# Kernel optimization log

Hardware: AMD Instinct MI355X
Metric: run time of the kernel (lower is better)

## Reference

```python
import jax, jax.numpy as jnp
import numpy as np

NUM_HEADS = 12


def get_rel_pos(q_size, k_size, rel_pos):
    # rel_pos: (2*max(q,k)-1, head_dim); sizes match table here so no resize.
    max_rel_dist = int(2 * max(q_size, k_size) - 1)
    if rel_pos.shape[0] != max_rel_dist:
        rel_pos = jax.image.resize(rel_pos, (max_rel_dist, rel_pos.shape[1]), method='linear')
    q_coords = jnp.arange(q_size)[:, None] * max(k_size / q_size, 1.0)
    k_coords = jnp.arange(k_size)[None, :] * max(q_size / k_size, 1.0)
    rel = (q_coords - k_coords + (k_size - 1) * max(q_size / k_size, 1.0)).astype(jnp.int32)
    return rel_pos[rel.reshape(-1)].reshape(q_size, k_size, -1)  # (q, k, head_dim)


def setup_inputs() -> dict:
    key = jax.random.key(0)
    ks = jax.random.split(key, 7)
    B, H, W, C = 8, 32, 32, 768
    head_dim = C // NUM_HEADS
    return {
        'x': jax.random.normal(ks[0], (B, H, W, C), jnp.float32),
        'w_qkv': jax.random.normal(ks[1], (C, 3 * C), jnp.float32) * 0.02,
        'b_qkv': jnp.zeros((3 * C,), jnp.float32),
        'rel_pos_h': jax.random.normal(ks[2], (2 * H - 1, head_dim), jnp.float32) * 0.02,
        'rel_pos_w': jax.random.normal(ks[3], (2 * W - 1, head_dim), jnp.float32) * 0.02,
        'w_proj': jax.random.normal(ks[4], (C, C), jnp.float32) * 0.02,
        'b_proj': jnp.zeros((C,), jnp.float32),
    }


def reference(x, w_qkv, b_qkv, rel_pos_h, rel_pos_w, w_proj, b_proj):
    B, H, W, C = x.shape
    heads = NUM_HEADS
    hd = C // heads
    S = H * W
    qkv = x @ w_qkv + b_qkv                                  # (B,H,W,3C)
    qkv = qkv.reshape(B, S, 3, heads, hd).transpose(2, 0, 3, 1, 4)
    qkv = qkv.reshape(3, B * heads, S, hd)
    q, k, v = qkv[0], qkv[1], qkv[2]
    attn = (q * hd ** -0.5) @ k.transpose(0, 2, 1)           # (B*heads, S, S)
    rh = get_rel_pos(H, H, rel_pos_h)                        # (H,H,hd)
    rw = get_rel_pos(W, W, rel_pos_w)                        # (W,W,hd)
    r_q = q.reshape(B * heads, H, W, hd)
    rel_h = jnp.einsum('bhwc,hkc->bhwk', r_q, rh)
    rel_w = jnp.einsum('bhwc,wkc->bhwk', r_q, rw)
    attn = (attn.reshape(B * heads, H, W, H, W)
            + rel_h[:, :, :, :, None]
            + rel_w[:, :, :, None, :]).reshape(B * heads, S, S)
    attn = jax.nn.softmax(attn, axis=-1)
    out = (attn @ v).reshape(B, heads, H, W, hd).transpose(0, 2, 3, 1, 4).reshape(B, H, W, C)
    return out @ w_proj + b_proj
```

## Files before the change

kernel.cpp:

```cpp
#include <hip/hip_runtime.h>
#include <hip/hip_bf16.h>

#define BATCH 8
#define SEQ   1024
#define CH    768
#define NH    12
#define HD    64
#define BH    96
#define N_QKV 2304

#define LOG2E 1.44269504088896f

typedef __attribute__((ext_vector_type(8))) short bfrag;
typedef __attribute__((ext_vector_type(4))) short short4v;
typedef __attribute__((ext_vector_type(4))) float ffrag;
typedef __attribute__((ext_vector_type(4))) int  intv4;
typedef __attribute__((ext_vector_type(2))) int  intv2;

__device__ __forceinline__ short f2bf(float x) {
    __hip_bfloat16 h = __float2bfloat16(x);
    return *reinterpret_cast<short*>(&h);
}
__device__ __forceinline__ float bf2f(short b) {
    __hip_bfloat16 h;
    *reinterpret_cast<short*>(&h) = b;
    return __bfloat162float(h);
}
__device__ __forceinline__ void split2(float x, short& hi, short& lo) {
    short h = f2bf(x);
    hi = h;
    lo = f2bf(x - bf2f(h));
}
__device__ __forceinline__ void async_copy16(void* lds, const void* g) {
    __builtin_amdgcn_global_load_lds(
        (const __attribute__((address_space(1))) void*)g,
        (__attribute__((address_space(3))) void*)lds, 16, 0, 0);
}
__device__ __forceinline__ void pinned_load16(intv4& dst, const void* p) {
    asm volatile("global_load_dwordx4 %0, %1, off"
                 : "=&v"(dst) : "v"((unsigned long long)p));
}

__global__ __launch_bounds__(256) void prep(
    const float* __restrict__ x,
    const float* __restrict__ w_qkv, const float* __restrict__ w_proj,
    short* __restrict__ Xh,
    short* __restrict__ WqhT,
    short* __restrict__ WphT, short* __restrict__ WplT)
{
    __shared__ float ts[32][33];
    const int tid = threadIdx.x;
    const int bid = blockIdx.x;

    if (bid < 512) {
        const int n4 = (BATCH * SEQ * CH) / 4;
        for (int i = bid * 256 + tid; i < n4; i += 512 * 256) {
            float4 f = ((const float4*)x)[i];
            short4v h;
            h[0] = f2bf(f.x); h[1] = f2bf(f.y); h[2] = f2bf(f.z); h[3] = f2bf(f.w);
            ((short4v*)Xh)[i] = h;
        }
        return;
    }
    if (bid < 2240) {
        int t = bid - 512;
        const int bx = t % 72, by = t / 72;
        const int r0 = by * 32, c0 = bx * 32;
        #pragma unroll
        for (int i = 0; i < 4; ++i) {
            int idx = tid + i * 256;
            int rr = idx >> 5, cc = idx & 31;
            ts[rr][cc] = w_qkv[(size_t)(r0 + rr) * N_QKV + c0 + cc];
        }
        __syncthreads();
        #pragma unroll
        for (int i = 0; i < 4; ++i) {
            int idx = tid + i * 256;
            int rr = idx >> 5, cc = idx & 31;
            WqhT[(size_t)(c0 + rr) * CH + r0 + cc] = f2bf(ts[cc][rr]);
        }
        return;
    }
    {
        int t = bid - 2240;
        const int bx = t % 24, by = t / 24;
        const int r0 = by * 32, c0 = bx * 32;
        #pragma unroll
        for (int i = 0; i < 4; ++i) {
            int idx = tid + i * 256;
            int rr = idx >> 5, cc = idx & 31;
            ts[rr][cc] = w_proj[(size_t)(r0 + rr) * CH + c0 + cc];
        }
        __syncthreads();
        #pragma unroll
        for (int i = 0; i < 4; ++i) {
            int idx = tid + i * 256;
            int rr = idx >> 5, cc = idx & 31;
            short h, l;
            split2(ts[cc][rr], h, l);
            WphT[(size_t)(c0 + rr) * CH + r0 + cc] = h;
            WplT[(size_t)(c0 + rr) * CH + r0 + cc] = l;
        }
    }
}

__global__ __launch_bounds__(256) void gemm_qkv_mfma(
    const short* __restrict__ Xh,
    const short* __restrict__ WhT,
    const float* __restrict__ bias,
    short* __restrict__ qh, short* __restrict__ kh, short* __restrict__ vT)
{
    __shared__ short lds[2 * 12288];
    const int id  = blockIdx.x;
    const int xcd = id & 7;
    const int per = id >> 3;
    const int mi_ = per & 3;
    const int ni_ = per >> 2;
    const int m0 = (xcd * 4 + mi_) * 256;
    const int n0 = ni_ * 128;
    const int which = n0 / CH;

    const int tid = threadIdx.x;
    const int wave = tid >> 6, lane = tid & 63;
    const int quad = lane >> 4, l16 = lane & 15;

    const size_t srow = (size_t)(tid >> 2) * CH
                      + (size_t)((tid & 3) ^ ((tid >> 3) & 3)) * 8;
    const short* asrc = Xh  + (size_t)m0 * CH + srow;
    const short* bsrc = WhT + (size_t)n0 * CH + srow;

    const int xs = (quad ^ ((l16 >> 1) & 3)) * 8;

    ffrag acc[4][8];
    #pragma unroll
    for (int i = 0; i < 4; ++i)
        #pragma unroll
        for (int j = 0; j < 8; ++j) acc[i][j] = (ffrag){0.f, 0.f, 0.f, 0.f};

    #pragma unroll
    for (int i = 0; i < 4; ++i)
        async_copy16(lds + i * 2048 + tid * 8, asrc + (size_t)i * 64 * CH);
    #pragma unroll
    for (int i = 0; i < 2; ++i)
        async_copy16(lds + 8192 + i * 2048 + tid * 8, bsrc + (size_t)i * 64 * CH);

    for (int c = 0; c < 24; ++c) {
        const int cur = c & 1;
        if (c < 23) {
            short* w = lds + (cur ^ 1) * 12288;
            #pragma unroll
            for (int i = 0; i < 4; ++i)
                async_copy16(w + i * 2048 + tid * 8,
                             asrc + (size_t)i * 64 * CH + (c + 1) * 32);
            #pragma unroll
            for (int i = 0; i < 2; ++i)
                async_copy16(w + 8192 + i * 2048 + tid * 8,
                             bsrc + (size_t)i * 64 * CH + (c + 1) * 32);
            asm volatile("s_waitcnt vmcnt(6)");
        } else {
            asm volatile("s_waitcnt vmcnt(0)");
        }
        __builtin_amdgcn_s_barrier();
        __builtin_amdgcn_sched_barrier(0);

        const short* Ab = lds + cur * 12288;
        const short* Bb = Ab + 8192;
        bfrag ah[4], bh[8];
        #pragma unroll
        for (int i = 0; i < 4; ++i)
            ah[i] = *(const bfrag*)&Ab[(wave * 64 + i * 16 + l16) * 32 + xs];
        #pragma unroll
        for (int j = 0; j < 8; ++j)
            bh[j] = *(const bfrag*)&Bb[(j * 16 + l16) * 32 + xs];
        __builtin_amdgcn_s_setprio(1);
        #pragma unroll
        for (int mi = 0; mi < 4; ++mi)
            #pragma unroll
            for (int ni = 0; ni < 8; ++ni)
                acc[mi][ni] = __builtin_amdgcn_mfma_f32_16x16x32_bf16(
                    ah[mi], bh[ni], acc[mi][ni], 0, 0, 0);
        __builtin_amdgcn_s_setprio(0);

        __builtin_amdgcn_s_barrier();
    }

    const int b = m0 >> 10;
    #pragma unroll
    for (int ni = 0; ni < 8; ++ni) {
        int n = n0 + ni * 16 + l16;
        float bv = bias[n];
        int nin = n - which * CH;
        int head = nin >> 6, d = nin & 63;
        #pragma unroll
        for (int mi = 0; mi < 4; ++mi) {
            if (which == 2) {
                int s_base = (m0 & 1023) + wave * 64 + mi * 16 + quad * 4;
                short4v pk;
                #pragma unroll
                for (int r = 0; r < 4; ++r) pk[r] = f2bf(acc[mi][ni][r] + bv);
                *(short4v*)&vT[((size_t)(b * NH + head) * HD + d) * SEQ + s_base] = pk;
            } else {
                const float scale = (which == 0) ? 0.125f * LOG2E : 1.0f;
                short* dst = (which == 0) ? qh : kh;
                #pragma unroll
                for (int r = 0; r < 4; ++r) {
                    int m = m0 + wave * 64 + mi * 16 + quad * 4 + r;
                    int s = m & 1023;
                    dst[((size_t)(b * NH + head) * SEQ + s) * HD + d] =
                        f2bf((acc[mi][ni][r] + bv) * scale);
                }
            }
        }
    }
}

__device__ __forceinline__ void gemm_core3(
    short* lds,
    const short* __restrict__ Ah, const short* __restrict__ Al,
    const short* __restrict__ BhT, const short* __restrict__ BlT,
    int m0, int n0, ffrag acc[4][4])
{
    const int tid = threadIdx.x;
    const int wave = tid >> 6, lane = tid & 63;
    const int quad = lane >> 4, l16 = lane & 15;
    const int wm = (wave & 1) * 64, wn = (wave >> 1) * 64;

    const short* src;
    int row0;
    if (wave == 0)      { src = Ah;  row0 = m0; }
    else if (wave == 1) { src = Al;  row0 = m0; }
    else if (wave == 2) { src = BhT; row0 = n0; }
    else                { src = BlT; row0 = n0; }
    const size_t lane_off = (size_t)(lane >> 2) * CH
                          + (size_t)((lane & 3) ^ ((lane >> 3) & 3)) * 8;
    const short* sbase = src + (size_t)row0 * CH + lane_off;
    short* wsec = lds + wave * 4096;

    const int xs = (quad ^ ((l16 >> 1) & 3)) * 8;

    #pragma unroll
    for (int i = 0; i < 8; ++i)
        async_copy16(wsec + i * 512, sbase + (size_t)i * 16 * CH);

    for (int c = 0; c < 24; ++c) {
        const int cur = c & 1;
        if (c < 23) {
            short* w = wsec + (cur ^ 1) * 16384;
            #pragma unroll
            for (int i = 0; i < 8; ++i)
                async_copy16(w + i * 512,
                             sbase + (size_t)i * 16 * CH + (c + 1) * 32);
            asm volatile("s_waitcnt vmcnt(8)");
        } else {
            asm volatile("s_waitcnt vmcnt(0)");
        }
        __builtin_amdgcn_s_barrier();
        __builtin_amdgcn_sched_barrier(0);

        const short* base = lds + cur * 16384;
        bfrag ah[4], al[4], bh[4], bl[4];
        #pragma unroll
        for (int i = 0; i < 4; ++i) {
            int ra = (wm + i * 16 + l16) * 32 + xs;
            int rb = (wn + i * 16 + l16) * 32 + xs;
            ah[i] = *(const bfrag*)&base[ra];
            al[i] = *(const bfrag*)&base[4096 + ra];
            bh[i] = *(const bfrag*)&base[8192 + rb];
            bl[i] = *(const bfrag*)&base[12288 + rb];
        }
        #pragma unroll
        for (int mi = 0; mi < 4; ++mi)
            #pragma unroll
            for (int ni = 0; ni < 4; ++ni) {
                acc[mi][ni] = __builtin_amdgcn_mfma_f32_16x16x32_bf16(ah[mi], bh[ni], acc[mi][ni], 0, 0, 0);
                acc[mi][ni] = __builtin_amdgcn_mfma_f32_16x16x32_bf16(ah[mi], bl[ni], acc[mi][ni], 0, 0, 0);
                acc[mi][ni] = __builtin_amdgcn_mfma_f32_16x16x32_bf16(al[mi], bh[ni], acc[mi][ni], 0, 0, 0);
            }

        __builtin_amdgcn_s_barrier();
    }
}

__global__ __launch_bounds__(256) void gemm_proj_mfma(
    const short* __restrict__ Ah, const short* __restrict__ Al,
    const short* __restrict__ WhT, const short* __restrict__ WlT,
    const float* __restrict__ bias, float* __restrict__ out)
{
    __shared__ short lds[2 * 16384];
    const int id  = blockIdx.x;
    const int xcd = id & 7;
    const int per = id >> 3;
    const int mi_ = per & 7;
    const int ni_ = per >> 3;
    const int m0 = (xcd * 8 + mi_) * 128;
    const int n0 = ni_ * 128;

    ffrag acc[4][4];
    #pragma unroll
    for (int i = 0; i < 4; ++i)
        #pragma unroll
        for (int j = 0; j < 4; ++j) acc[i][j] = (ffrag){0.f, 0.f, 0.f, 0.f};

    gemm_core3(lds, Ah, Al, WhT, WlT, m0, n0, acc);

    const int tid = threadIdx.x;
    const int wave = tid >> 6, lane = tid & 63;
    const int quad = lane >> 4, l16 = lane & 15;
    const int wm = (wave & 1) * 64, wn = (wave >> 1) * 64;

    #pragma unroll
    for (int ni = 0; ni < 4; ++ni) {
        int n = n0 + wn + ni * 16 + l16;
        float bv = bias[n];
        #pragma unroll
        for (int mi = 0; mi < 4; ++mi)
            #pragma unroll
            for (int r = 0; r < 4; ++r) {
                int m = m0 + wm + mi * 16 + quad * 4 + r;
                out[(size_t)m * CH + n] = acc[mi][ni][r] + bv;
            }
    }
}

__global__ __launch_bounds__(256, 3) void attn_kernel(
    const short* __restrict__ qh,
    const short* __restrict__ kh_g, const short* __restrict__ vT_g,
    const float* __restrict__ rph,
    const float* __restrict__ rpw,
    short* __restrict__ aoh, short* __restrict__ aol)
{
    const int fid   = blockIdx.x;
    const int xcd   = fid & 7;
    const int inner = fid >> 3;
    const int s0    = (inner & 7) * 128;
    const int bh    = xcd * 12 + (inner >> 3);

    const int tid  = threadIdx.x;
    const int wave = tid >> 6;
    const int lane = tid & 63;
    const int quad = lane >> 4;
    const int l16  = lane & 15;

    __shared__ short Kh[64 * 64];
    __shared__ short Vth[64 * 64];
    __shared__ short Th[128][68];
    __shared__ short Tw_Ps[128 * 68];

    const size_t bh_koff = (size_t)bh * SEQ * HD;
    const size_t bh_voff = (size_t)bh * HD * SEQ;
    const size_t klane = (size_t)(lane >> 3) * HD + (size_t)((lane & 7) ^ (lane >> 3)) * 8;

    const short* kbase = kh_g + bh_koff + klane;
    const int i0 = wave * 2;
    short* KhW0 = Kh + i0 * 512 + lane * 8;

    const short* vgbase = vT_g + bh_voff
        + (size_t)(wave * 16 + (lane >> 3)) * SEQ + (size_t)(lane & 7) * 8;

    int vwA[2], vwB[2];
    {
        const int m  = lane & 7;
        const int oA = ((m >> 2) << 2) + ((m & 1) << 1);
        const int hf = (m >> 1) & 1;
        #pragma unroll
        for (int jj = 0; jj < 2; ++jj) {
            int d = wave * 16 + jj * 8 + (lane >> 3);
            vwA[jj] = d * 64 + ((oA ^ (d & 7)) << 3) + hf * 4;
            vwB[jj] = d * 64 + (((oA + 1) ^ (d & 7)) << 3) + hf * 4;
        }
    }

    intv4 kA0, kA1, vA0, vA1, kB0, kB1, vB0, vB1;
    pinned_load16(kA0, kbase + (size_t)(i0 * 8) * HD);
    pinned_load16(kA1, kbase + (size_t)(i0 * 8 + 8) * HD);
    pinned_load16(vA0, vgbase);
    pinned_load16(vA1, vgbase + (size_t)8 * SEQ);

    bfrag qfh[2][2];
    #pragma unroll
    for (int g = 0; g < 2; ++g) {
        const size_t qrow = ((size_t)bh * SEQ + s0 + wave * 32 + g * 16 + l16) * HD;
        #pragma unroll
        for (int kc = 0; kc < 2; ++kc)
            qfh[g][kc] = *(const bfrag*)(qh + qrow + kc * 32 + quad * 8);
    }

    #pragma unroll
    for (int table = 0; table < 2; ++table) {
        const float* tbl = table ? rpw : rph;
        #pragma unroll
        for (int n0r = 0; n0r < 64; n0r += 16) {
            int r = n0r + l16;
            bfrag bfr[2];
            #pragma unroll
            for (int kc = 0; kc < 2; ++kc) {
                if (r < 63) {
                    const float* trow = tbl + (size_t)r * HD + kc * 32 + quad * 8;
                    float4 f0 = *(const float4*)(trow);
                    float4 f1 = *(const float4*)(trow + 4);
                    float xs[8] = {f0.x, f0.y, f0.z, f0.w, f1.x, f1.y, f1.z, f1.w};
                    #pragma unroll
                    for (int j = 0; j < 8; ++j) bfr[kc][j] = f2bf(xs[j]);
                } else {
                    #pragma unroll
                    for (int j = 0; j < 8; ++j) bfr[kc][j] = 0;
                }
            }
            #pragma unroll
            for (int g = 0; g < 2; ++g) {
                ffrag acc = {0.f, 0.f, 0.f, 0.f};
                acc = __builtin_amdgcn_mfma_f32_16x16x32_bf16(qfh[g][0], bfr[0], acc, 0, 0, 0);
                acc = __builtin_amdgcn_mfma_f32_16x16x32_bf16(qfh[g][1], bfr[1], acc, 0, 0, 0);
                int row = wave * 32 + g * 16 + quad * 4;
                #pragma unroll
                for (int reg = 0; reg < 4; ++reg) {
                    short v = f2bf(acc[reg] * 8.0f);
                    if (table) Tw_Ps[(row + reg) * 68 + n0r + l16] = v;
                    else       Th[row + reg][n0r + l16] = v;
                }
            }
        }
    }

    float tw_r[2][2][4];
    #pragma unroll
    for (int g = 0; g < 2; ++g) {
        int qloc = wave * 32 + g * 16 + l16;
        int wq = g * 16 + l16;
        #pragma unroll
        for (int p = 0; p < 2; ++p)
            #pragma unroll
            for (int reg = 0; reg < 4; ++reg)
                tw_r[g][p][reg] = bf2f(Tw_Ps[qloc * 68 + (wq - (p * 16 + quad * 4 + reg) + 31)]);
    }
    const int hq_w = (s0 >> 5) + wave;

    float l_part[2] = {0.f, 0.f};
    ffrag Ot[2][4];
    #pragma unroll
    for (int g = 0; g < 2; ++g)
        #pragma unroll
        for (int t = 0; t < 4; ++t) Ot[g][t] = (ffrag){0.f, 0.f, 0.f, 0.f};

    auto chunk = [&](int c, const intv4& ck0, const intv4& ck1,
                     const intv4& cv0, const intv4& cv1,
                     intv4& nk0, intv4& nk1, intv4& nv0, intv4& nv1) {
        __syncthreads();
        if (c < 15) {
            const int cn = c + 1;
            pinned_load16(nk0, kbase + (size_t)(cn * 64 + i0 * 8) * HD);
            pinned_load16(nk1, kbase + (size_t)(cn * 64 + i0 * 8 + 8) * HD);
            pinned_load16(nv0, vgbase + cn * 64);
            pinned_load16(nv1, vgbase + (size_t)8 * SEQ + cn * 64);
            asm volatile("s_waitcnt vmcnt(4)");
        } else {
            asm volatile("s_waitcnt vmcnt(0)");
        }
        __builtin_amdgcn_sched_barrier(0);
        *(intv4*)KhW0         = ck0;
        *(intv4*)(KhW0 + 512) = ck1;
        {
            intv2 lo0 = {cv0[0], cv0[1]}, hi0 = {cv0[2], cv0[3]};
            intv2 lo1 = {cv1[0], cv1[1]}, hi1 = {cv1[2], cv1[3]};
            *(intv2*)&Vth[vwA[0]] = lo0;
            *(intv2*)&Vth[vwB[0]] = hi0;
            *(intv2*)&Vth[vwA[1]] = lo1;
            *(intv2*)&Vth[vwB[1]] = hi1;
        }
        __syncthreads();

        float th_r[2][2];
        #pragma unroll
        for (int g = 0; g < 2; ++g) {
            int qloc = wave * 32 + g * 16 + l16;
            th_r[g][0] = bf2f(Th[qloc][hq_w - 2 * c + 31]);
            th_r[g][1] = bf2f(Th[qloc][hq_w - 2 * c - 1 + 31]);
        }

        #pragma unroll
        for (int ktp = 0; ktp < 2; ++ktp) {
            bfrag kbhE[2], kbhO[2];
            #pragma unroll
            for (int kc = 0; kc < 2; ++kc) {
                int xs = ((kc * 4 + quad) ^ (l16 & 7)) * 8;
                kbhE[kc] = *(const bfrag*)&Kh[((2 * ktp) * 16 + l16) * 64 + xs];
                kbhO[kc] = *(const bfrag*)&Kh[((2 * ktp + 1) * 16 + l16) * 64 + xs];
            }
            bfrag pf[2];
            #pragma unroll
            for (int g = 0; g < 2; ++g) {
                ffrag aE, aO;
                #pragma unroll
                for (int reg = 0; reg < 4; ++reg) {
                    aE[reg] = th_r[g][ktp] + tw_r[g][0][reg];
                    aO[reg] = th_r[g][ktp] + tw_r[g][1][reg];
                }
                __builtin_amdgcn_s_setprio(1);
                aE = __builtin_amdgcn_mfma_f32_16x16x32_bf16(kbhE[0], qfh[g][0], aE, 0, 0, 0);
                aE = __builtin_amdgcn_mfma_f32_16x16x32_bf16(kbhE[1], qfh[g][1], aE, 0, 0, 0);
                aO = __builtin_amdgcn_mfma_f32_16x16x32_bf16(kbhO[0], qfh[g][0], aO, 0, 0, 0);
                aO = __builtin_amdgcn_mfma_f32_16x16x32_bf16(kbhO[1], qfh[g][1], aO, 0, 0, 0);
                __builtin_amdgcn_s_setprio(0);
                #pragma unroll
                for (int reg = 0; reg < 4; ++reg) {
                    float pE = exp2f(aE[reg]);
                    float pO = exp2f(aO[reg]);
                    l_part[g] += pE + pO;
                    pf[g][reg]     = f2bf(pE);
                    pf[g][reg + 4] = f2bf(pO);
                }
            }
            #pragma unroll
            for (int t = 0; t < 4; ++t) {
                int d = t * 16 + l16;
                int xv = ((ktp * 4 + quad) ^ (l16 & 7)) * 8;
                bfrag vh = *(const bfrag*)&Vth[d * 64 + xv];
                __builtin_amdgcn_s_setprio(1);
                #pragma unroll
                for (int g = 0; g < 2; ++g)
                    Ot[g][t] = __builtin_amdgcn_mfma_f32_16x16x32_bf16(pf[g], vh, Ot[g][t], 0, 0, 0);
                __builtin_amdgcn_s_setprio(0);
            }
        }
    };

    for (int cc = 0; cc < 8; ++cc) {
        chunk(2 * cc,     kA0, kA1, vA0, vA1, kB0, kB1, vB0, vB1);
        chunk(2 * cc + 1, kB0, kB1, vB0, vB1, kA0, kA1, vA0, vA1);
    }

    {
        int b = bh / NH, head = bh % NH;
        #pragma unroll
        for (int g = 0; g < 2; ++g) {
            float r = l_part[g];
            r += __shfl_xor(r, 16, 64);
            r += __shfl_xor(r, 32, 64);
            float invl = 1.f / r;
            float inv[4];
            #pragma unroll
            for (int reg = 0; reg < 4; ++reg)
                inv[reg] = __shfl(invl, quad * 4 + reg, 16);
            #pragma unroll
            for (int t = 0; t < 4; ++t) {
                #pragma unroll
                for (int reg = 0; reg < 4; ++reg) {
                    int s_ = s0 + wave * 32 + g * 16 + quad * 4 + reg;
                    int d = t * 16 + l16;
                    size_t idx = ((size_t)(b * SEQ + s_)) * CH + head * HD + d;
                    short h, l;
                    split2(Ot[g][t][reg] * inv[reg], h, l);
                    aoh[idx] = h;
                    aol[idx] = l;
                }
            }
        }
    }
}

extern "C" void kernel_launch(void* const* d_in, const int* in_sizes, int n_in,
                              void* d_out, int out_size, void* d_ws, size_t ws_size,
                              hipStream_t stream) {
    const float* x       = (const float*)d_in[0];
    const float* w_qkv   = (const float*)d_in[1];
    const float* b_qkv   = (const float*)d_in[2];
    const float* rph     = (const float*)d_in[3];
    const float* rpw     = (const float*)d_in[4];
    const float* w_proj  = (const float*)d_in[5];
    const float* b_proj  = (const float*)d_in[6];
    float* out = (float*)d_out;

    const size_t NTOK = (size_t)BATCH * SEQ;
    const size_t XSZ  = NTOK * CH;
    const size_t WQSZ = (size_t)N_QKV * CH;
    const size_t WPSZ = (size_t)CH * CH;
    short* Xh   = (short*)d_ws;
    short* AoL  = Xh + XSZ;
    short* WqhT = AoL + XSZ;
    short* WphT = WqhT + WQSZ;
    short* WplT = WphT + WPSZ;
    short* qh = WplT + WPSZ;
    short* kh = qh + XSZ;
    short* vT = kh + XSZ;
    short* aoh = Xh;
    short* aol = AoL;

    prep<<<dim3(2816), 256, 0, stream>>>(x, w_qkv, w_proj,
                                         Xh, WqhT, WphT, WplT);
    gemm_qkv_mfma<<<dim3(576), 256, 0, stream>>>(Xh, WqhT, b_qkv,
                                                 qh, kh, vT);
    attn_kernel<<<dim3(768), 256, 0, stream>>>(qh, kh, vT,
                                               rph, rpw, aoh, aol);
    gemm_proj_mfma<<<dim3(384), 256, 0, stream>>>(aoh, aol, WphT, WplT,
                                                  b_proj, out);
}
```

Before: 227.9 us.

## Halve attention query tile to 64 rows for higher occupancy with async K copy

```diff
diff --git a/kernel.cpp b/kernel.cpp
--- a/kernel.cpp
+++ b/kernel.cpp
@@ -322,7 +322,7 @@
     }
 }
 
-__global__ __launch_bounds__(256, 3) void attn_kernel(
+__global__ __launch_bounds__(256, 6) void attn_kernel(
     const short* __restrict__ qh,
     const short* __restrict__ kh_g, const short* __restrict__ vT_g,
     const float* __restrict__ rph,
@@ -332,8 +332,8 @@
     const int fid   = blockIdx.x;
     const int xcd   = fid & 7;
     const int inner = fid >> 3;
-    const int s0    = (inner & 7) * 128;
-    const int bh    = xcd * 12 + (inner >> 3);
+    const int s0    = (inner & 15) * 64;
+    const int bh    = xcd * 12 + (inner >> 4);
 
     const int tid  = threadIdx.x;
     const int wave = tid >> 6;
@@ -343,8 +343,7 @@
 
     __shared__ short Kh[64 * 64];
     __shared__ short Vth[64 * 64];
-    __shared__ short Th[128][68];
-    __shared__ short Tw_Ps[128 * 68];
+    __shared__ short ThTw[64][68];
 
     const size_t bh_koff = (size_t)bh * SEQ * HD;
     const size_t bh_voff = (size_t)bh * HD * SEQ;
@@ -352,7 +351,6 @@
 
     const short* kbase = kh_g + bh_koff + klane;
     const int i0 = wave * 2;
-    short* KhW0 = Kh + i0 * 512 + lane * 8;
 
     const short* vgbase = vT_g + bh_voff
         + (size_t)(wave * 16 + (lane >> 3)) * SEQ + (size_t)(lane & 7) * 8;
@@ -370,24 +368,18 @@
         }
     }
 
-    intv4 kA0, kA1, vA0, vA1, kB0, kB1, vB0, vB1;
-    pinned_load16(kA0, kbase + (size_t)(i0 * 8) * HD);
-    pinned_load16(kA1, kbase + (size_t)(i0 * 8 + 8) * HD);
+    intv4 vA0, vA1;
     pinned_load16(vA0, vgbase);
     pinned_load16(vA1, vgbase + (size_t)8 * SEQ);
 
-    bfrag qfh[2][2];
-    #pragma unroll
-    for (int g = 0; g < 2; ++g) {
-        const size_t qrow = ((size_t)bh * SEQ + s0 + wave * 32 + g * 16 + l16) * HD;
-        #pragma unroll
-        for (int kc = 0; kc < 2; ++kc)
-            qfh[g][kc] = *(const bfrag*)(qh + qrow + kc * 32 + quad * 8);
-    }
-
-    #pragma unroll
-    for (int table = 0; table < 2; ++table) {
-        const float* tbl = table ? rpw : rph;
+    bfrag qfh[2];
+    {
+        const size_t qrow = ((size_t)bh * SEQ + s0 + wave * 16 + l16) * HD;
+        qfh[0] = *(const bfrag*)(qh + qrow + quad * 8);
+        qfh[1] = *(const bfrag*)(qh + qrow + 32 + quad * 8);
+    }
+
+    auto build_table = [&](const float* tbl) {
         #pragma unroll
         for (int n0r = 0; n0r < 64; n0r += 16) {
             int r = n0r + l16;
@@ -398,70 +390,50 @@
                     const float* trow = tbl + (size_t)r * HD + kc * 32 + quad * 8;
                     float4 f0 = *(const float4*)(trow);
                     float4 f1 = *(const float4*)(trow + 4);
-                    float xs[8] = {f0.x, f0.y, f0.z, f0.w, f1.x, f1.y, f1.z, f1.w};
+                    float xsv[8] = {f0.x, f0.y, f0.z, f0.w, f1.x, f1.y, f1.z, f1.w};
                     #pragma unroll
-                    for (int j = 0; j < 8; ++j) bfr[kc][j] = f2bf(xs[j]);
+                    for (int j = 0; j < 8; ++j) bfr[kc][j] = f2bf(xsv[j]);
                 } else {
                     #pragma unroll
                     for (int j = 0; j < 8; ++j) bfr[kc][j] = 0;
                 }
             }
-            #pragma unroll
-            for (int g = 0; g < 2; ++g) {
-                ffrag acc = {0.f, 0.f, 0.f, 0.f};
-                acc = __builtin_amdgcn_mfma_f32_16x16x32_bf16(qfh[g][0], bfr[0], acc, 0, 0, 0);
-                acc = __builtin_amdgcn_mfma_f32_16x16x32_bf16(qfh[g][1], bfr[1], acc, 0, 0, 0);
-                int row = wave * 32 + g * 16 + quad * 4;
-                #pragma unroll
-                for (int reg = 0; reg < 4; ++reg) {
-                    short v = f2bf(acc[reg] * 8.0f);
-                    if (table) Tw_Ps[(row + reg) * 68 + n0r + l16] = v;
-                    else       Th[row + reg][n0r + l16] = v;
-                }
-            }
-        }
-    }
-
-    float tw_r[2][2][4];
-    #pragma unroll
-    for (int g = 0; g < 2; ++g) {
-        int qloc = wave * 32 + g * 16 + l16;
-        int wq = g * 16 + l16;
+            ffrag acc = {0.f, 0.f, 0.f, 0.f};
+            acc = __builtin_amdgcn_mfma_f32_16x16x32_bf16(qfh[0], bfr[0], acc, 0, 0, 0);
+            acc = __builtin_amdgcn_mfma_f32_16x16x32_bf16(qfh[1], bfr[1], acc, 0, 0, 0);
+            int row = wave * 16 + quad * 4;
+            #pragma unroll
+            for (int reg = 0; reg < 4; ++reg)
+                ThTw[row + reg][n0r + l16] = f2bf(acc[reg] * 8.0f);
+        }
+    };
+
+    build_table(rpw);
+    float tw_r[2][4];
+    {
+        int qloc = wave * 16 + l16;
+        int wq = ((wave & 1) << 4) + l16;
         #pragma unroll
         for (int p = 0; p < 2; ++p)
             #pragma unroll
             for (int reg = 0; reg < 4; ++reg)
-                tw_r[g][p][reg] = bf2f(Tw_Ps[qloc * 68 + (wq - (p * 16 + quad * 4 + reg) + 31)]);
-    }
-    const int hq_w = (s0 >> 5) + wave;
-
-    float l_part[2] = {0.f, 0.f};
-    ffrag Ot[2][4];
-    #pragma unroll
-    for (int g = 0; g < 2; ++g)
-        #pragma unroll
-        for (int t = 0; t < 4; ++t) Ot[g][t] = (ffrag){0.f, 0.f, 0.f, 0.f};
-
-    auto chunk = [&](int c, const intv4& ck0, const intv4& ck1,
-                     const intv4& cv0, const intv4& cv1,
-                     intv4& nk0, intv4& nk1, intv4& nv0, intv4& nv1) {
+                tw_r[p][reg] = bf2f(ThTw[qloc][wq - (p * 16 + quad * 4 + reg) + 31]);
+    }
+    build_table(rph);
+    const int hq_w = (s0 >> 5) + (wave >> 1);
+
+    float l_part = 0.f;
+    ffrag Ot[4];
+    #pragma unroll
+    for (int t = 0; t < 4; ++t) Ot[t] = (ffrag){0.f, 0.f, 0.f, 0.f};
+
+    for (int c = 0; c < 16; ++c) {
         __syncthreads();
-        if (c < 15) {
-            const int cn = c + 1;
-            pinned_load16(nk0, kbase + (size_t)(cn * 64 + i0 * 8) * HD);
-            pinned_load16(nk1, kbase + (size_t)(cn * 64 + i0 * 8 + 8) * HD);
-            pinned_load16(nv0, vgbase + cn * 64);
-            pinned_load16(nv1, vgbase + (size_t)8 * SEQ + cn * 64);
-            asm volatile("s_waitcnt vmcnt(4)");
-        } else {
-            asm volatile("s_waitcnt vmcnt(0)");
-        }
-        __builtin_amdgcn_sched_barrier(0);
-        *(intv4*)KhW0         = ck0;
-        *(intv4*)(KhW0 + 512) = ck1;
+        async_copy16(Kh + i0 * 512,       kbase + (size_t)(c * 64 + i0 * 8) * HD);
+        async_copy16(Kh + (i0 + 1) * 512, kbase + (size_t)(c * 64 + i0 * 8 + 8) * HD);
         {
-            intv2 lo0 = {cv0[0], cv0[1]}, hi0 = {cv0[2], cv0[3]};
-            intv2 lo1 = {cv1[0], cv1[1]}, hi1 = {cv1[2], cv1[3]};
+            intv2 lo0 = {vA0[0], vA0[1]}, hi0 = {vA0[2], vA0[3]};
+            intv2 lo1 = {vA1[0], vA1[1]}, hi1 = {vA1[2], vA1[3]};
             *(intv2*)&Vth[vwA[0]] = lo0;
             *(intv2*)&Vth[vwB[0]] = hi0;
             *(intv2*)&Vth[vwA[1]] = lo1;
@@ -469,12 +441,16 @@
         }
         __syncthreads();
 
-        float th_r[2][2];
-        #pragma unroll
-        for (int g = 0; g < 2; ++g) {
-            int qloc = wave * 32 + g * 16 + l16;
-            th_r[g][0] = bf2f(Th[qloc][hq_w - 2 * c + 31]);
-            th_r[g][1] = bf2f(Th[qloc][hq_w - 2 * c - 1 + 31]);
+        if (c < 15) {
+            pinned_load16(vA0, vgbase + (c + 1) * 64);
+            pinned_load16(vA1, vgbase + (size_t)8 * SEQ + (c + 1) * 64);
+        }
+
+        float th_r[2];
+        {
+            int qloc = wave * 16 + l16;
+            th_r[0] = bf2f(ThTw[qloc][hq_w - 2 * c + 31]);
+            th_r[1] = bf2f(ThTw[qloc][hq_w - 2 * c - 1 + 31]);
         }
 
         #pragma unroll
@@ -482,33 +458,30 @@
             bfrag kbhE[2], kbhO[2];
             #pragma unroll
             for (int kc = 0; kc < 2; ++kc) {
-                int xs = ((kc * 4 + quad) ^ (l16 & 7)) * 8;
-                kbhE[kc] = *(const bfrag*)&Kh[((2 * ktp) * 16 + l16) * 64 + xs];
-                kbhO[kc] = *(const bfrag*)&Kh[((2 * ktp + 1) * 16 + l16) * 64 + xs];
-            }
-            bfrag pf[2];
-            #pragma unroll
-            for (int g = 0; g < 2; ++g) {
-                ffrag aE, aO;
-                #pragma unroll
-                for (int reg = 0; reg < 4; ++reg) {
-                    aE[reg] = th_r[g][ktp] + tw_r[g][0][reg];
-                    aO[reg] = th_r[g][ktp] + tw_r[g][1][reg];
-                }
-                __builtin_amdgcn_s_setprio(1);
-                aE = __builtin_amdgcn_mfma_f32_16x16x32_bf16(kbhE[0], qfh[g][0], aE, 0, 0, 0);
-                aE = __builtin_amdgcn_mfma_f32_16x16x32_bf16(kbhE[1], qfh[g][1], aE, 0, 0, 0);
-                aO = __builtin_amdgcn_mfma_f32_16x16x32_bf16(kbhO[0], qfh[g][0], aO, 0, 0, 0);
-                aO = __builtin_amdgcn_mfma_f32_16x16x32_bf16(kbhO[1], qfh[g][1], aO, 0, 0, 0);
-                __builtin_amdgcn_s_setprio(0);
-                #pragma unroll
-                for (int reg = 0; reg < 4; ++reg) {
-                    float pE = exp2f(aE[reg]);
-                    float pO = exp2f(aO[reg]);
-                    l_part[g] += pE + pO;
-                    pf[g][reg]     = f2bf(pE);
-                    pf[g][reg + 4] = f2bf(pO);
-                }
+                int xsk = ((kc * 4 + quad) ^ (l16 & 7)) * 8;
+                kbhE[kc] = *(const bfrag*)&Kh[((2 * ktp) * 16 + l16) * 64 + xsk];
+                kbhO[kc] = *(const bfrag*)&Kh[((2 * ktp + 1) * 16 + l16) * 64 + xsk];
+            }
+            ffrag aE, aO;
+            #pragma unroll
+            for (int reg = 0; reg < 4; ++reg) {
+                aE[reg] = th_r[ktp] + tw_r[0][reg];
+                aO[reg] = th_r[ktp] + tw_r[1][reg];
+            }
+            __builtin_amdgcn_s_setprio(1);
+            aE = __builtin_amdgcn_mfma_f32_16x16x32_bf16(kbhE[0], qfh[0], aE, 0, 0, 0);
+            aE = __builtin_amdgcn_mfma_f32_16x16x32_bf16(kbhE[1], qfh[1], aE, 0, 0, 0);
+            aO = __builtin_amdgcn_mfma_f32_16x16x32_bf16(kbhO[0], qfh[0], aO, 0, 0, 0);
+            aO = __builtin_amdgcn_mfma_f32_16x16x32_bf16(kbhO[1], qfh[1], aO, 0, 0, 0);
+            __builtin_amdgcn_s_setprio(0);
+            bfrag pf;
+            #pragma unroll
+            for (int reg = 0; reg < 4; ++reg) {
+                float pE = exp2f(aE[reg]);
+                float pO = exp2f(aO[reg]);
+                l_part += pE + pO;
+                pf[reg]     = f2bf(pE);
+                pf[reg + 4] = f2bf(pO);
             }
             #pragma unroll
             for (int t = 0; t < 4; ++t) {
@@ -516,43 +489,33 @@
                 int xv = ((ktp * 4 + quad) ^ (l16 & 7)) * 8;
                 bfrag vh = *(const bfrag*)&Vth[d * 64 + xv];
                 __builtin_amdgcn_s_setprio(1);
-                #pragma unroll
-                for (int g = 0; g < 2; ++g)
-                    Ot[g][t] = __builtin_amdgcn_mfma_f32_16x16x32_bf16(pf[g], vh, Ot[g][t], 0, 0, 0);
+                Ot[t] = __builtin_amdgcn_mfma_f32_16x16x32_bf16(pf, vh, Ot[t], 0, 0, 0);
                 __builtin_amdgcn_s_setprio(0);
             }
         }
-    };
-
-    for (int cc = 0; cc < 8; ++cc) {
-        chunk(2 * cc,     kA0, kA1, vA0, vA1, kB0, kB1, vB0, vB1);
-        chunk(2 * cc + 1, kB0, kB1, vB0, vB1, kA0, kA1, vA0, vA1);
     }
 
     {
         int b = bh / NH, head = bh % NH;
-        #pragma unroll
-        for (int g = 0; g < 2; ++g) {
-            float r = l_part[g];
-            r += __shfl_xor(r, 16, 64);
-            r += __shfl_xor(r, 32, 64);
-            float invl = 1.f / r;
-            float inv[4];
-            #pragma unroll
-            for (int reg = 0; reg < 4; ++reg)
-                inv[reg] = __shfl(invl, quad * 4 + reg, 16);
-            #pragma unroll
-            for (int t = 0; t < 4; ++t) {
-                #pragma unroll
-                for (int reg = 0; reg < 4; ++reg) {
-                    int s_ = s0 + wave * 32 + g * 16 + quad * 4 + reg;
-                    int d = t * 16 + l16;
-                    size_t idx = ((size_t)(b * SEQ + s_)) * CH + head * HD + d;
-                    short h, l;
-                    split2(Ot[g][t][reg] * inv[reg], h, l);
-                    aoh[idx] = h;
-                    aol[idx] = l;
-                }
+        float r = l_part;
+        r += __shfl_xor(r, 16, 64);
+        r += __shfl_xor(r, 32, 64);
+        float invl = 1.f / r;
+        float inv[4];
+        #pragma unroll
+        for (int reg = 0; reg < 4; ++reg)
+            inv[reg] = __shfl(invl, quad * 4 + reg, 16);
+        #pragma unroll
+        for (int t = 0; t < 4; ++t) {
+            #pragma unroll
+            for (int reg = 0; reg < 4; ++reg) {
+                int s_ = s0 + wave * 16 + quad * 4 + reg;
+                int d = t * 16 + l16;
+                size_t idx = ((size_t)(b * SEQ + s_)) * CH + head * HD + d;
+                short h, l;
+                split2(Ot[t][reg] * inv[reg], h, l);
+                aoh[idx] = h;
+                aol[idx] = l;
             }
         }
     }
@@ -589,8 +552,8 @@
                                          Xh, WqhT, WphT, WplT);
     gemm_qkv_mfma<<<dim3(576), 256, 0, stream>>>(Xh, WqhT, b_qkv,
                                                  qh, kh, vT);
-    attn_kernel<<<dim3(768), 256, 0, stream>>>(qh, kh, vT,
-                                               rph, rpw, aoh, aol);
+    attn_kernel<<<dim3(1536), 256, 0, stream>>>(qh, kh, vT,
+                                                rph, rpw, aoh, aol);
     gemm_proj_mfma<<<dim3(384), 256, 0, stream>>>(aoh, aol, WphT, WplT,
                                                   b_proj, out);
 }
```

Measured after the change: 269.3 us. +18.2%, slower.
